# Performance work log

Measured on AMD Instinct MI355X. Metric: run time of the kernel, lower is better.

## Reference

```python
import jax, jax.numpy as jnp
import numpy as np

B, N, T, H, O = 4, 100, 20, 64, 128


def setup_inputs() -> dict:
    key = jax.random.key(0)
    ks = jax.random.split(key, 21)
    def rn(k, shape, scale=0.05):
        return jax.random.normal(k, shape, jnp.float32) * scale
    return dict(
        edge_weights=jax.random.uniform(ks[0], (B, N, N, T), jnp.float32),
        W_edge=rn(ks[1], (1, H)), b_edge=rn(ks[2], (H,)),
        conv1_w=rn(ks[3], (H, H, 3)), conv1_b=rn(ks[4], (H,)),
        conv2_w=rn(ks[5], (H, H, 3)), conv2_b=rn(ks[6], (H,)),
        Wt1=rn(ks[7], (H, H)), bt1=rn(ks[8], (H,)),
        Wt2=rn(ks[9], (H, 1)), bt2=rn(ks[10], (1,)),
        Ws1=rn(ks[11], (H, H)), bs1=rn(ks[12], (H,)),
        Ws2=rn(ks[13], (H, 1)), bs2=rn(ks[14], (1,)),
        Wg1=rn(ks[15], (H, H)), bg1=rn(ks[16], (H,)),
        Wg2=rn(ks[17], (H, H)), bg2=rn(ks[18], (H,)),
        Wout=rn(ks[19], (H, O)), bout=rn(ks[20], (O,)),
    )


def _conv1d(x, w, b):
    # x: [M, C, T], w: [Cout, Cin, 3], padding=1 (same)
    y = jax.lax.conv_general_dilated(x, w, window_strides=(1,), padding=[(1, 1)],
                                     dimension_numbers=('NCH', 'OIH', 'NCH'))
    return y + b[None, :, None]


def reference(edge_weights, W_edge, b_edge, conv1_w, conv1_b, conv2_w, conv2_b,
              Wt1, bt1, Wt2, bt2, Ws1, bs1, Ws2, bs2, Wg1, bg1, Wg2, bg2,
              Wout, bout):
    b, n, _, t = edge_weights.shape
    h = W_edge.shape[1]
    # edge embedding: Linear(1, H) on trailing scalar -> [B,N,N,T,H]
    ef = edge_weights[..., None] * W_edge[0] + b_edge
    # temporal conv block over T
    xr = ef.reshape(b * n * n, t, h).transpose(0, 2, 1)           # [M,H,T]
    xr = jax.nn.relu(_conv1d(xr, conv1_w, conv1_b))
    xr = jax.nn.relu(_conv1d(xr, conv2_w, conv2_b))
    xc = xr.transpose(0, 2, 1)                                     # [M,T,H]
    # temporal attention over T
    u = jnp.tanh(xc @ Wt1 + bt1)
    att_t = jax.nn.softmax((u @ Wt2 + bt2)[..., 0], axis=1)        # [M,T]
    efa = jnp.sum(xc * att_t[..., None], axis=1).reshape(b, n, n, h)  # [B,N,N,H]
    # spatial attention over all N*N edges
    us = jnp.tanh(efa.reshape(b, n * n, h) @ Ws1 + bs1)
    att_s = jax.nn.softmax((us @ Ws2 + bs2)[..., 0], axis=1).reshape(b, n, n)
    node = jnp.sum(efa * att_s[..., None], axis=2)                 # [B,N,H]
    node = jax.nn.relu(node @ Wg1 + bg1)
    node = jax.nn.relu(node @ Wg2 + bg2)
    # output projection (Dropout is identity in eval)
    node_emb = jax.nn.relu(node @ Wout + bout)                     # [B,N,O]
    return node_emb
```

## Files before the change

kernel.cpp:

```cpp
#include <hip/hip_runtime.h>
#include <math.h>

#define BN 4
#define NNODE 100
#define TT 20
#define HH 64
#define OO 128
#define M (BN*NNODE*NNODE)
#define EPB 2

#define WS_A1   0
#define WS_C3   192
#define WS_W2F  384
#define WS_WT1F (WS_W2F + 6144)
#define WS_WS1F (WS_WT1F + 2048)
#define WS_EFA  (WS_WS1F + 2048)
#define WS_ESC  (WS_EFA + M*32)

typedef _Float16 half8 __attribute__((ext_vector_type(8)));
typedef _Float16 half4 __attribute__((ext_vector_type(4)));
typedef float float4v __attribute__((ext_vector_type(4)));

__global__ void prep_kernel(const float* __restrict__ W_edge,
                            const float* __restrict__ b_edge,
                            const float* __restrict__ w1,
                            const float* __restrict__ b1,
                            const float* __restrict__ w2,
                            const float* __restrict__ Wt1,
                            const float* __restrict__ Ws1,
                            float* __restrict__ ws)
{
    const int tid  = blockIdx.x * blockDim.x + threadIdx.x;
    const int nthr = gridDim.x * blockDim.x;
    if (tid < 64) {
        int co = tid;
        float a[3] = {0.f, 0.f, 0.f};
        float bk[3] = {0.f, 0.f, 0.f};
        for (int ci = 0; ci < HH; ++ci) {
            float we = W_edge[ci], be = b_edge[ci];
#pragma unroll
            for (int k = 0; k < 3; ++k) {
                float w = w1[(co*HH + ci)*3 + k];
                a[k]  = fmaf(we, w, a[k]);
                bk[k] = fmaf(be, w, bk[k]);
            }
        }
        float bb = b1[co];
        ws[WS_A1 + 0*64 + co] = a[0];
        ws[WS_A1 + 1*64 + co] = a[1];
        ws[WS_A1 + 2*64 + co] = a[2];
        ws[WS_C3 +        co] = bb + bk[1] + bk[2];
        ws[WS_C3 +  64 +  co] = bb + bk[0] + bk[1] + bk[2];
        ws[WS_C3 + 128 +  co] = bb + bk[0] + bk[1];
    }
    _Float16* w2f  = (_Float16*)(ws + WS_W2F);
    _Float16* wt1f = (_Float16*)(ws + WS_WT1F);
    _Float16* ws1f = (_Float16*)(ws + WS_WS1F);
    for (int s = tid; s < 24*64*8; s += nthr) {
        int j    = s & 7;
        int lane = (s >> 3) & 63;
        int f    = s >> 9;
        int mt = f / 6, kt = f % 6;
        int co = mt*16 + (lane & 15);
        int q  = kt*32 + ((lane >> 4) << 3) + j;
        int k  = q >> 6, ci = q & 63;
        w2f[f*512 + lane*8 + j] = (_Float16)w2[(co*HH + ci)*3 + k];
    }
    for (int s = tid; s < 8*64*8; s += nthr) {
        int j    = s & 7;
        int lane = (s >> 3) & 63;
        int f    = s >> 9;
        int kt = f / 4, nt = f % 4;
        int ci = kt*32 + ((lane >> 4) << 3) + j;
        int co = nt*16 + (lane & 15);
        wt1f[f*512 + lane*8 + j] = (_Float16)Wt1[ci*HH + co];
        ws1f[f*512 + lane*8 + j] = (_Float16)Ws1[ci*HH + co];
    }
}

__launch_bounds__(EPB*64)
__global__ void edge_kernel(const float* __restrict__ ew_g,
                            const float* __restrict__ ws_c,
                            const float* __restrict__ b2,
                            const float* __restrict__ bt1,
                            const float* __restrict__ Wt2,
                            const float* __restrict__ bt2,
                            const float* __restrict__ bs1,
                            const float* __restrict__ Ws2,
                            const float* __restrict__ bs2,
                            _Float16* __restrict__ efa_g,
                            float* __restrict__ score_g)
{
    __shared__ _Float16 y1p[EPB][22*72];
    __shared__ _Float16 y2L[EPB][TT*72];
    __shared__ float    sbuf[EPB][TT];
    __shared__ float    ewp[EPB][22];

    const int w    = threadIdx.x >> 6;
    const int lane = threadIdx.x & 63;
    const int m    = blockIdx.x * EPB + w;
    const int l15  = lane & 15;
    const int quad = lane >> 4;

    if (lane < TT)      ewp[w][lane + 1] = ew_g[m*TT + lane];
    else if (lane < 22) ewp[w][(lane - TT) * 21] = 0.f;

    const float a0 = ws_c[WS_A1 +       lane];
    const float a1 = ws_c[WS_A1 +  64 + lane];
    const float a2 = ws_c[WS_A1 + 128 + lane];
    const float c0 = ws_c[WS_C3 +       lane];
    const float cf = ws_c[WS_C3 +  64 + lane];
    const float cL = ws_c[WS_C3 + 128 + lane];

    y1p[w][lane] = (_Float16)0.f;
    y1p[w][21*72 + lane] = (_Float16)0.f;
#pragma unroll
    for (int t = 0; t < TT; ++t) {
        float c = (t == 0) ? c0 : (t == TT-1) ? cL : cf;
        float v = fmaf(a0, ewp[w][t], fmaf(a1, ewp[w][t+1], fmaf(a2, ewp[w][t+2], c)));
        y1p[w][(t+1)*72 + lane] = (_Float16)fmaxf(v, 0.f);
    }

    const _Float16* w2f = (const _Float16*)(ws_c + WS_W2F);
    float4v acc[4][2];
#pragma unroll
    for (int mt = 0; mt < 4; ++mt)
#pragma unroll
        for (int nt = 0; nt < 2; ++nt)
            acc[mt][nt] = float4v{0.f, 0.f, 0.f, 0.f};

    const int tB0 = l15;
    const int tB1 = (16 + l15 < TT) ? (16 + l15) : TT-1;
#pragma unroll
    for (int kt = 0; kt < 6; ++kt) {
        const int cofs = (kt & 1)*32 + quad*8;
        const int rofs = (kt >> 1);
        half8 b0 = *(const half8*)&y1p[w][(tB0 + rofs)*72 + cofs];
        half8 b1 = *(const half8*)&y1p[w][(tB1 + rofs)*72 + cofs];
#pragma unroll
        for (int mt = 0; mt < 4; ++mt) {
            half8 a = *(const half8*)(w2f + ((mt*6 + kt)*64 + lane)*8);
            acc[mt][0] = __builtin_amdgcn_mfma_f32_16x16x32_f16(a, b0, acc[mt][0], 0, 0, 0);
            acc[mt][1] = __builtin_amdgcn_mfma_f32_16x16x32_f16(a, b1, acc[mt][1], 0, 0, 0);
        }
    }
#pragma unroll
    for (int mt = 0; mt < 4; ++mt) {
        const float4v bb = *(const float4v*)&b2[mt*16 + quad*4];
        half4 h0;
#pragma unroll
        for (int reg = 0; reg < 4; ++reg)
            h0[reg] = (_Float16)fmaxf(acc[mt][0][reg] + bb[reg], 0.f);
        *(half4*)&y2L[w][l15*72 + mt*16 + quad*4] = h0;
        if (l15 < TT - 16) {
            half4 h1;
#pragma unroll
            for (int reg = 0; reg < 4; ++reg)
                h1[reg] = (_Float16)fmaxf(acc[mt][1][reg] + bb[reg], 0.f);
            *(half4*)&y2L[w][(16 + l15)*72 + mt*16 + quad*4] = h1;
        }
    }

    const _Float16* wt1f = (const _Float16*)(ws_c + WS_WT1F);
    float4v u[2][4];
#pragma unroll
    for (int mt = 0; mt < 2; ++mt)
#pragma unroll
        for (int nt = 0; nt < 4; ++nt)
            u[mt][nt] = float4v{0.f, 0.f, 0.f, 0.f};
#pragma unroll
    for (int kt = 0; kt < 2; ++kt) {
        half8 af0 = *(const half8*)&y2L[w][tB0*72 + kt*32 + quad*8];
        half8 af1 = *(const half8*)&y2L[w][tB1*72 + kt*32 + quad*8];
#pragma unroll
        for (int nt = 0; nt < 4; ++nt) {
            half8 bf = *(const half8*)(wt1f + ((kt*4 + nt)*64 + lane)*8);
            u[0][nt] = __builtin_amdgcn_mfma_f32_16x16x32_f16(af0, bf, u[0][nt], 0, 0, 0);
            u[1][nt] = __builtin_amdgcn_mfma_f32_16x16x32_f16(af1, bf, u[1][nt], 0, 0, 0);
        }
    }

    float bt1v[4], wt2v[4];
#pragma unroll
    for (int nt = 0; nt < 4; ++nt) {
        bt1v[nt] = bt1[nt*16 + l15];
        wt2v[nt] = Wt2[nt*16 + l15];
    }
#pragma unroll
    for (int mt = 0; mt < 2; ++mt) {
#pragma unroll
        for (int reg = 0; reg < 4; ++reg) {
            int t = mt*16 + quad*4 + reg;
            float p = 0.f;
#pragma unroll
            for (int nt = 0; nt < 4; ++nt) {
                float x  = u[mt][nt][reg] + bt1v[nt];
                float x2 = x * x;
                float q  = fmaf(x2, -0.053968254f, 0.13333333f);
                q = fmaf(q, x2, -0.33333333f);
                q = fmaf(q, x2, 1.f);
                p = fmaf(x * q, wt2v[nt], p);
            }
            p += __shfl_xor(p, 1, 64);
            p += __shfl_xor(p, 2, 64);
            p += __shfl_xor(p, 4, 64);
            p += __shfl_xor(p, 8, 64);
            if (l15 == 0 && t < TT) sbuf[w][t] = p;
        }
    }

    float ev = (lane < TT) ? __expf(sbuf[w][lane] + bt2[0]) : 0.f;
    float sum = ev;
#pragma unroll
    for (int off = 32; off >= 1; off >>= 1)
        sum += __shfl_xor(sum, off, 64);
    float inv = __fdividef(1.f, sum);

    float e0 = 0.f, e1 = 0.f, e2 = 0.f, e3 = 0.f;
#pragma unroll
    for (int t = 0; t < TT; t += 4) {
        e0 = fmaf((float)y2L[w][(t+0)*72 + lane], __shfl(ev, t+0, 64), e0);
        e1 = fmaf((float)y2L[w][(t+1)*72 + lane], __shfl(ev, t+1, 64), e1);
        e2 = fmaf((float)y2L[w][(t+2)*72 + lane], __shfl(ev, t+2, 64), e2);
        e3 = fmaf((float)y2L[w][(t+3)*72 + lane], __shfl(ev, t+3, 64), e3);
    }
    float efa = ((e0 + e1) + (e2 + e3)) * inv;
    efa_g[m*64 + lane] = (_Float16)efa;

    y1p[w][lane] = (_Float16)efa;
    half8 ea0 = *(const half8*)&y1p[w][quad*8];
    half8 ea1 = *(const half8*)&y1p[w][32 + quad*8];
    const _Float16* ws1f = (const _Float16*)(ws_c + WS_WS1F);
    float4v uv[4];
#pragma unroll
    for (int nt = 0; nt < 4; ++nt) uv[nt] = float4v{0.f, 0.f, 0.f, 0.f};
#pragma unroll
    for (int nt = 0; nt < 4; ++nt) {
        half8 bf0 = *(const half8*)(ws1f + ((0*4 + nt)*64 + lane)*8);
        half8 bf1 = *(const half8*)(ws1f + ((1*4 + nt)*64 + lane)*8);
        uv[nt] = __builtin_amdgcn_mfma_f32_16x16x32_f16(ea0, bf0, uv[nt], 0, 0, 0);
        uv[nt] = __builtin_amdgcn_mfma_f32_16x16x32_f16(ea1, bf1, uv[nt], 0, 0, 0);
    }
    float p = 0.f;
#pragma unroll
    for (int nt = 0; nt < 4; ++nt) {
        float x = uv[nt][0] + bs1[nt*16 + l15];
        float x2 = x * x;
        p = fmaf(x * (15.f + x2),
                 __fdividef(Ws2[nt*16 + l15], fmaf(6.f, x2, 15.f)), p);
    }
    p += __shfl_xor(p, 1, 64);
    p += __shfl_xor(p, 2, 64);
    p += __shfl_xor(p, 4, 64);
    p += __shfl_xor(p, 8, 64);
    if (lane == 0)
        score_g[m] = __expf(p + bs2[0]);
}

__launch_bounds__(256)
__global__ void node_kernel(const _Float16* __restrict__ efa_g,
                            const float* __restrict__ e_g,
                            const float* __restrict__ Wg1,
                            const float* __restrict__ bg1,
                            const float* __restrict__ Wg2,
                            const float* __restrict__ bg2,
                            const float* __restrict__ Wout,
                            const float* __restrict__ bout,
                            float* __restrict__ out)
{
    __shared__ float part[4][64];
    __shared__ float red[256];
    const int bi   = blockIdx.x;
    const int b    = bi / NNODE;
    const int tid  = threadIdx.x;
    const int lane = tid & 63;
    const int w    = tid >> 6;
    const int base = bi * NNODE;

    float dsum = 0.f;
    for (int i = tid; i < NNODE*NNODE; i += 256)
        dsum += e_g[b*NNODE*NNODE + i];
    red[tid] = dsum; __syncthreads();
    for (int s = 128; s >= 1; s >>= 1) {
        if (tid < s) red[tid] += red[tid + s];
        __syncthreads();
    }
    const float invden = __fdividef(1.f, red[0]);

    float acc0 = 0.f, acc1 = 0.f;
    for (int j = w; j < NNODE; j += 8) {
        acc0 = fmaf(e_g[base + j], (float)efa_g[(base + j)*64 + lane], acc0);
        int j2 = j + 4;
        if (j2 < NNODE)
            acc1 = fmaf(e_g[base + j2], (float)efa_g[(base + j2)*64 + lane], acc1);
    }
    part[w][lane] = acc0 + acc1;
    __syncthreads();
    if (w != 0) return;

    float node = (part[0][lane] + part[1][lane] + part[2][lane] + part[3][lane]) * invden;

    float a0 = bg1[lane], a1 = 0.f, a2 = 0.f, a3 = 0.f;
#pragma unroll
    for (int ci = 0; ci < HH; ci += 4) {
        a0 = fmaf(__shfl(node, ci + 0, 64), Wg1[(ci + 0)*HH + lane], a0);
        a1 = fmaf(__shfl(node, ci + 1, 64), Wg1[(ci + 1)*HH + lane], a1);
        a2 = fmaf(__shfl(node, ci + 2, 64), Wg1[(ci + 2)*HH + lane], a2);
        a3 = fmaf(__shfl(node, ci + 3, 64), Wg1[(ci + 3)*HH + lane], a3);
    }
    float g1 = fmaxf((a0 + a1) + (a2 + a3), 0.f);

    a0 = bg2[lane]; a1 = 0.f; a2 = 0.f; a3 = 0.f;
#pragma unroll
    for (int ci = 0; ci < HH; ci += 4) {
        a0 = fmaf(__shfl(g1, ci + 0, 64), Wg2[(ci + 0)*HH + lane], a0);
        a1 = fmaf(__shfl(g1, ci + 1, 64), Wg2[(ci + 1)*HH + lane], a1);
        a2 = fmaf(__shfl(g1, ci + 2, 64), Wg2[(ci + 2)*HH + lane], a2);
        a3 = fmaf(__shfl(g1, ci + 3, 64), Wg2[(ci + 3)*HH + lane], a3);
    }
    float g2 = fmaxf((a0 + a1) + (a2 + a3), 0.f);

    float o0 = bout[lane], o1 = bout[lane + 64];
    float q0 = 0.f, q1 = 0.f;
#pragma unroll
    for (int ci = 0; ci < HH; ci += 2) {
        float ga = __shfl(g2, ci, 64), gb = __shfl(g2, ci + 1, 64);
        o0 = fmaf(ga, Wout[ci*OO + lane],            o0);
        o1 = fmaf(ga, Wout[ci*OO + lane + 64],       o1);
        q0 = fmaf(gb, Wout[(ci + 1)*OO + lane],      q0);
        q1 = fmaf(gb, Wout[(ci + 1)*OO + lane + 64], q1);
    }
    out[bi*OO + lane]      = fmaxf(o0 + q0, 0.f);
    out[bi*OO + lane + 64] = fmaxf(o1 + q1, 0.f);
}

extern "C" void kernel_launch(void* const* d_in, const int* in_sizes, int n_in,
                              void* d_out, int out_size, void* d_ws, size_t ws_size,
                              hipStream_t stream)
{
    const float* ew      = (const float*)d_in[0];
    const float* W_edge  = (const float*)d_in[1];
    const float* b_edge  = (const float*)d_in[2];
    const float* conv1_w = (const float*)d_in[3];
    const float* conv1_b = (const float*)d_in[4];
    const float* conv2_w = (const float*)d_in[5];
    const float* conv2_b = (const float*)d_in[6];
    const float* Wt1     = (const float*)d_in[7];
    const float* bt1     = (const float*)d_in[8];
    const float* Wt2     = (const float*)d_in[9];
    const float* bt2     = (const float*)d_in[10];
    const float* Ws1     = (const float*)d_in[11];
    const float* bs1     = (const float*)d_in[12];
    const float* Ws2     = (const float*)d_in[13];
    const float* bs2     = (const float*)d_in[14];
    const float* Wg1     = (const float*)d_in[15];
    const float* bg1     = (const float*)d_in[16];
    const float* Wg2     = (const float*)d_in[17];
    const float* bg2     = (const float*)d_in[18];
    const float* Wout    = (const float*)d_in[19];
    const float* bout    = (const float*)d_in[20];

    float* ws  = (float*)d_ws;
    float* out = (float*)d_out;
    _Float16* efa_h = (_Float16*)(ws + WS_EFA);

    prep_kernel<<<16, 256, 0, stream>>>(W_edge, b_edge, conv1_w, conv1_b, conv2_w,
                                        Wt1, Ws1, ws);

    edge_kernel<<<M/EPB, EPB*64, 0, stream>>>(ew, ws, conv2_b,
                                              bt1, Wt2, bt2,
                                              bs1, Ws2, bs2,
                                              efa_h, ws + WS_ESC);

    node_kernel<<<BN*NNODE, 256, 0, stream>>>(efa_h, ws + WS_ESC,
                                              Wg1, bg1, Wg2, bg2, Wout, bout, out);
}
```

Before: 210.0 us.

## Pack four edges per wavefront to fill MFMA tiles without padding waste

Each 64-lane wavefront now processes four edges instead of one. The 80 time-step rows (4 edges × 20) are packed into five full 16-row MFMA tiles, so the old padded second tile that held only 4 valid rows is gone. Weight fragments for the temporal attention are loaded once and reused across the five tiles. The conv2 output overwrites the conv1 LDS buffer in place, and the spatial-attention MFMA covers four edges at once. In exchange, each wave holds more accumulator registers (20 float4 tiles), which could lower occupancy, and rows are mapped to (edge, time) with a divide-by-multiply trick.

New measurement: 196.5 us. 6.4% less time.

```diff
diff --git a/kernel.cpp b/kernel.cpp
--- a/kernel.cpp
+++ b/kernel.cpp
@@ -7,7 +7,6 @@
 #define HH 64
 #define OO 128
 #define M (BN*NNODE*NNODE)
-#define EPB 2
 
 #define WS_A1   0
 #define WS_C3   192
@@ -78,7 +77,7 @@
     }
 }
 
-__launch_bounds__(EPB*64)
+__launch_bounds__(64)
 __global__ void edge_kernel(const float* __restrict__ ew_g,
                             const float* __restrict__ ws_c,
                             const float* __restrict__ b2,
@@ -91,19 +90,27 @@
                             _Float16* __restrict__ efa_g,
                             float* __restrict__ score_g)
 {
-    __shared__ _Float16 y1p[EPB][22*72];
-    __shared__ _Float16 y2L[EPB][TT*72];
-    __shared__ float    sbuf[EPB][TT];
-    __shared__ float    ewp[EPB][22];
-
-    const int w    = threadIdx.x >> 6;
-    const int lane = threadIdx.x & 63;
-    const int m    = blockIdx.x * EPB + w;
+    __shared__ _Float16 y1s[4*1584];
+    __shared__ float    sbuf[4][20];
+    __shared__ float    ewp[4][22];
+
+    const int lane = threadIdx.x;
+    const int m0   = blockIdx.x * 4;
     const int l15  = lane & 15;
     const int quad = lane >> 4;
 
-    if (lane < TT)      ewp[w][lane + 1] = ew_g[m*TT + lane];
-    else if (lane < 22) ewp[w][(lane - TT) * 21] = 0.f;
+    {
+        float v = ew_g[m0*TT + lane];
+        int e = (lane*205) >> 12; int t = lane - e*20;
+        ewp[e][t + 1] = v;
+        if (lane < 16) {
+            int c2 = 64 + lane;
+            float v2 = ew_g[m0*TT + c2];
+            int e2 = (c2*205) >> 12; int t2 = c2 - e2*20;
+            ewp[e2][t2 + 1] = v2;
+        }
+        if (lane < 4) { ewp[lane][0] = 0.f; ewp[lane][21] = 0.f; }
+    }
 
     const float a0 = ws_c[WS_A1 +       lane];
     const float a1 = ws_c[WS_A1 +  64 + lane];
@@ -112,73 +119,76 @@
     const float cf = ws_c[WS_C3 +  64 + lane];
     const float cL = ws_c[WS_C3 + 128 + lane];
 
-    y1p[w][lane] = (_Float16)0.f;
-    y1p[w][21*72 + lane] = (_Float16)0.f;
-#pragma unroll
-    for (int t = 0; t < TT; ++t) {
-        float c = (t == 0) ? c0 : (t == TT-1) ? cL : cf;
-        float v = fmaf(a0, ewp[w][t], fmaf(a1, ewp[w][t+1], fmaf(a2, ewp[w][t+2], c)));
-        y1p[w][(t+1)*72 + lane] = (_Float16)fmaxf(v, 0.f);
+#pragma unroll
+    for (int e = 0; e < 4; ++e) {
+        y1s[e*1584 + lane] = (_Float16)0.f;
+        y1s[e*1584 + 21*72 + lane] = (_Float16)0.f;
+#pragma unroll
+        for (int t = 0; t < TT; ++t) {
+            float c = (t == 0) ? c0 : (t == TT-1) ? cL : cf;
+            float v = fmaf(a0, ewp[e][t], fmaf(a1, ewp[e][t+1], fmaf(a2, ewp[e][t+2], c)));
+            y1s[e*1584 + (t+1)*72 + lane] = (_Float16)fmaxf(v, 0.f);
+        }
+    }
+
+    int baddr[5], ce[5], ct[5];
+#pragma unroll
+    for (int n = 0; n < 5; ++n) {
+        int c = n*16 + l15;
+        int e = (c*205) >> 12;
+        int t = c - e*20;
+        ce[n] = e; ct[n] = t;
+        baddr[n] = e*1584 + t*72 + quad*8;
     }
 
     const _Float16* w2f = (const _Float16*)(ws_c + WS_W2F);
-    float4v acc[4][2];
+    float4v acc[4][5];
 #pragma unroll
     for (int mt = 0; mt < 4; ++mt)
 #pragma unroll
-        for (int nt = 0; nt < 2; ++nt)
-            acc[mt][nt] = float4v{0.f, 0.f, 0.f, 0.f};
-
-    const int tB0 = l15;
-    const int tB1 = (16 + l15 < TT) ? (16 + l15) : TT-1;
+        for (int n = 0; n < 5; ++n)
+            acc[mt][n] = float4v{0.f, 0.f, 0.f, 0.f};
+
 #pragma unroll
     for (int kt = 0; kt < 6; ++kt) {
-        const int cofs = (kt & 1)*32 + quad*8;
-        const int rofs = (kt >> 1);
-        half8 b0 = *(const half8*)&y1p[w][(tB0 + rofs)*72 + cofs];
-        half8 b1 = *(const half8*)&y1p[w][(tB1 + rofs)*72 + cofs];
+        const int koff = (kt >> 1)*72 + (kt & 1)*32;
+        half8 b[5];
+#pragma unroll
+        for (int n = 0; n < 5; ++n)
+            b[n] = *(const half8*)&y1s[baddr[n] + koff];
 #pragma unroll
         for (int mt = 0; mt < 4; ++mt) {
             half8 a = *(const half8*)(w2f + ((mt*6 + kt)*64 + lane)*8);
-            acc[mt][0] = __builtin_amdgcn_mfma_f32_16x16x32_f16(a, b0, acc[mt][0], 0, 0, 0);
-            acc[mt][1] = __builtin_amdgcn_mfma_f32_16x16x32_f16(a, b1, acc[mt][1], 0, 0, 0);
-        }
-    }
-#pragma unroll
-    for (int mt = 0; mt < 4; ++mt) {
-        const float4v bb = *(const float4v*)&b2[mt*16 + quad*4];
-        half4 h0;
-#pragma unroll
-        for (int reg = 0; reg < 4; ++reg)
-            h0[reg] = (_Float16)fmaxf(acc[mt][0][reg] + bb[reg], 0.f);
-        *(half4*)&y2L[w][l15*72 + mt*16 + quad*4] = h0;
-        if (l15 < TT - 16) {
-            half4 h1;
+#pragma unroll
+            for (int n = 0; n < 5; ++n)
+                acc[mt][n] = __builtin_amdgcn_mfma_f32_16x16x32_f16(a, b[n], acc[mt][n], 0, 0, 0);
+        }
+    }
+
+    float4v bb[4];
+#pragma unroll
+    for (int mt = 0; mt < 4; ++mt)
+        bb[mt] = *(const float4v*)&b2[mt*16 + quad*4];
+#pragma unroll
+    for (int n = 0; n < 5; ++n) {
+        const int ybase = ce[n]*1584 + ct[n]*72;
+#pragma unroll
+        for (int mt = 0; mt < 4; ++mt) {
+            half4 h;
 #pragma unroll
             for (int reg = 0; reg < 4; ++reg)
-                h1[reg] = (_Float16)fmaxf(acc[mt][1][reg] + bb[reg], 0.f);
-            *(half4*)&y2L[w][(16 + l15)*72 + mt*16 + quad*4] = h1;
+                h[reg] = (_Float16)fmaxf(acc[mt][n][reg] + bb[mt][reg], 0.f);
+            *(half4*)&y1s[ybase + mt*16 + quad*4] = h;
         }
     }
 
     const _Float16* wt1f = (const _Float16*)(ws_c + WS_WT1F);
-    float4v u[2][4];
-#pragma unroll
-    for (int mt = 0; mt < 2; ++mt)
+    half8 bf[2][4];
+#pragma unroll
+    for (int kt = 0; kt < 2; ++kt)
 #pragma unroll
         for (int nt = 0; nt < 4; ++nt)
-            u[mt][nt] = float4v{0.f, 0.f, 0.f, 0.f};
-#pragma unroll
-    for (int kt = 0; kt < 2; ++kt) {
-        half8 af0 = *(const half8*)&y2L[w][tB0*72 + kt*32 + quad*8];
-        half8 af1 = *(const half8*)&y2L[w][tB1*72 + kt*32 + quad*8];
-#pragma unroll
-        for (int nt = 0; nt < 4; ++nt) {
-            half8 bf = *(const half8*)(wt1f + ((kt*4 + nt)*64 + lane)*8);
-            u[0][nt] = __builtin_amdgcn_mfma_f32_16x16x32_f16(af0, bf, u[0][nt], 0, 0, 0);
-            u[1][nt] = __builtin_amdgcn_mfma_f32_16x16x32_f16(af1, bf, u[1][nt], 0, 0, 0);
-        }
-    }
+            bf[kt][nt] = *(const half8*)(wt1f + ((kt*4 + nt)*64 + lane)*8);
 
     float bt1v[4], wt2v[4];
 #pragma unroll
@@ -186,15 +196,29 @@
         bt1v[nt] = bt1[nt*16 + l15];
         wt2v[nt] = Wt2[nt*16 + l15];
     }
-#pragma unroll
-    for (int mt = 0; mt < 2; ++mt) {
+
+#pragma unroll
+    for (int mtile = 0; mtile < 5; ++mtile) {
+        int r = mtile*16 + l15;
+        int e = (r*205) >> 12; int t = r - e*20;
+        const int abase = e*1584 + t*72 + quad*8;
+        float4v u[4];
+#pragma unroll
+        for (int nt = 0; nt < 4; ++nt) u[nt] = float4v{0.f, 0.f, 0.f, 0.f};
+#pragma unroll
+        for (int kt = 0; kt < 2; ++kt) {
+            half8 af = *(const half8*)&y1s[abase + kt*32];
+#pragma unroll
+            for (int nt = 0; nt < 4; ++nt)
+                u[nt] = __builtin_amdgcn_mfma_f32_16x16x32_f16(af, bf[kt][nt], u[nt], 0, 0, 0);
+        }
 #pragma unroll
         for (int reg = 0; reg < 4; ++reg) {
-            int t = mt*16 + quad*4 + reg;
+            int rr = mtile*16 + quad*4 + reg;
             float p = 0.f;
 #pragma unroll
             for (int nt = 0; nt < 4; ++nt) {
-                float x  = u[mt][nt][reg] + bt1v[nt];
+                float x  = u[nt][reg] + bt1v[nt];
                 float x2 = x * x;
                 float q  = fmaf(x2, -0.053968254f, 0.13333333f);
                 q = fmaf(q, x2, -0.33333333f);
@@ -205,31 +229,46 @@
             p += __shfl_xor(p, 2, 64);
             p += __shfl_xor(p, 4, 64);
             p += __shfl_xor(p, 8, 64);
-            if (l15 == 0 && t < TT) sbuf[w][t] = p;
-        }
-    }
-
-    float ev = (lane < TT) ? __expf(sbuf[w][lane] + bt2[0]) : 0.f;
-    float sum = ev;
-#pragma unroll
-    for (int off = 32; off >= 1; off >>= 1)
-        sum += __shfl_xor(sum, off, 64);
+            if (l15 == 0) {
+                int ee = (rr*205) >> 12;
+                sbuf[ee][rr - ee*20] = p;
+            }
+        }
+    }
+
+    const float bt2v = bt2[0];
+    float ev1 = __expf(sbuf[quad][l15] + bt2v);
+    float ev2 = (l15 < 4) ? __expf(sbuf[quad][16 + l15] + bt2v) : 0.f;
+    float sum = ev1 + ev2;
+    sum += __shfl_xor(sum, 1, 64);
+    sum += __shfl_xor(sum, 2, 64);
+    sum += __shfl_xor(sum, 4, 64);
+    sum += __shfl_xor(sum, 8, 64);
     float inv = __fdividef(1.f, sum);
-
-    float e0 = 0.f, e1 = 0.f, e2 = 0.f, e3 = 0.f;
-#pragma unroll
-    for (int t = 0; t < TT; t += 4) {
-        e0 = fmaf((float)y2L[w][(t+0)*72 + lane], __shfl(ev, t+0, 64), e0);
-        e1 = fmaf((float)y2L[w][(t+1)*72 + lane], __shfl(ev, t+1, 64), e1);
-        e2 = fmaf((float)y2L[w][(t+2)*72 + lane], __shfl(ev, t+2, 64), e2);
-        e3 = fmaf((float)y2L[w][(t+3)*72 + lane], __shfl(ev, t+3, 64), e3);
-    }
-    float efa = ((e0 + e1) + (e2 + e3)) * inv;
-    efa_g[m*64 + lane] = (_Float16)efa;
-
-    y1p[w][lane] = (_Float16)efa;
-    half8 ea0 = *(const half8*)&y1p[w][quad*8];
-    half8 ea1 = *(const half8*)&y1p[w][32 + quad*8];
+    sbuf[quad][l15] = ev1 * inv;
+    if (l15 < 4) sbuf[quad][16 + l15] = ev2 * inv;
+
+    float efav[4];
+#pragma unroll
+    for (int e = 0; e < 4; ++e) {
+        const int yb = e*1584;
+        float p0 = 0.f, p1 = 0.f, p2 = 0.f, p3 = 0.f;
+#pragma unroll
+        for (int t = 0; t < TT; t += 4) {
+            p0 = fmaf((float)y1s[yb + (t+0)*72 + lane], sbuf[e][t+0], p0);
+            p1 = fmaf((float)y1s[yb + (t+1)*72 + lane], sbuf[e][t+1], p1);
+            p2 = fmaf((float)y1s[yb + (t+2)*72 + lane], sbuf[e][t+2], p2);
+            p3 = fmaf((float)y1s[yb + (t+3)*72 + lane], sbuf[e][t+3], p3);
+        }
+        efav[e] = (p0 + p1) + (p2 + p3);
+        efa_g[(m0 + e)*64 + lane] = (_Float16)efav[e];
+    }
+
+#pragma unroll
+    for (int e = 0; e < 4; ++e)
+        y1s[e*64 + lane] = (_Float16)efav[e];
+    half8 ea0 = *(const half8*)&y1s[(l15 >> 2)*64 + quad*8];
+    half8 ea1 = *(const half8*)&y1s[(l15 >> 2)*64 + 32 + quad*8];
     const _Float16* ws1f = (const _Float16*)(ws_c + WS_WS1F);
     float4v uv[4];
 #pragma unroll
@@ -253,8 +292,8 @@
     p += __shfl_xor(p, 2, 64);
     p += __shfl_xor(p, 4, 64);
     p += __shfl_xor(p, 8, 64);
-    if (lane == 0)
-        score_g[m] = __expf(p + bs2[0]);
+    if (l15 == 0)
+        score_g[m0 + quad] = __expf(p + bs2[0]);
 }
 
 __launch_bounds__(256)
@@ -367,10 +406,10 @@
     prep_kernel<<<16, 256, 0, stream>>>(W_edge, b_edge, conv1_w, conv1_b, conv2_w,
                                         Wt1, Ws1, ws);
 
-    edge_kernel<<<M/EPB, EPB*64, 0, stream>>>(ew, ws, conv2_b,
-                                              bt1, Wt2, bt2,
-                                              bs1, Ws2, bs2,
-                                              efa_h, ws + WS_ESC);
+    edge_kernel<<<M/4, 64, 0, stream>>>(ew, ws, conv2_b,
+                                        bt1, Wt2, bt2,
+                                        bs1, Ws2, bs2,
+                                        efa_h, ws + WS_ESC);
 
     node_kernel<<<BN*NNODE, 256, 0, stream>>>(efa_h, ws + WS_ESC,
                                               Wg1, bg1, Wg2, bg2, Wout, bout, out);
```
